# Kernel optimization log

Hardware: AMD Instinct MI355X
Metric: run time of the kernel (lower is better)

Reference implementation:

```python
import jax, jax.numpy as jnp
import numpy as np

B, S, H = 128, 1024, 256
NEG = 1e9

def setup_inputs() -> dict:
    key = jax.random.key(0)
    ks = jax.random.split(key, 11)
    sc = 0.05
    return {
        'ref': jax.random.normal(ks[0], (B, S, H), jnp.float32),
        'query': jax.random.normal(ks[1], (B, H), jnp.float32),
        'mask': jax.random.randint(ks[2], (B, S), 0, 2, jnp.int32),
        'wg': jax.random.normal(ks[3], (H, H), jnp.float32) * sc,
        'bg': jax.random.normal(ks[4], (H,), jnp.float32) * sc,
        'wqg': jax.random.normal(ks[5], (H, H), jnp.float32) * sc,
        'vg': jax.random.normal(ks[6], (H,), jnp.float32) * sc,
        'wp': jax.random.normal(ks[7], (H, H), jnp.float32) * sc,
        'bp': jax.random.normal(ks[8], (H,), jnp.float32) * sc,
        'wqp': jax.random.normal(ks[9], (H, H), jnp.float32) * sc,
        'vp': jax.random.normal(ks[10], (H,), jnp.float32) * sc,
    }

def reference(ref, query, mask, wg, bg, wqg, vg, wp, bp, wqp, vp):
    # Bahdanau additive pointer attention with glimpse, per PointerDecoder.pointer_net
    maskf = mask.astype(ref.dtype)
    # glimpse attention
    enc_g = jnp.einsum('bsd,hd->bsh', ref, wg) + bg            # conv1d kernel=1
    q_g = jnp.einsum('bd,hd->bh', query, wqg)                   # w_q_g (no bias)
    scores_g = jnp.einsum('bsh,h->bs', jnp.tanh(enc_g + q_g[:, None, :]), vg)
    att_g = jax.nn.softmax(scores_g - maskf * NEG, axis=-1)     # [B,S]
    glimpse = jnp.einsum('bs,bsd->bd', att_g, ref) + query      # [B,H]
    # pointer scores
    enc_p = jnp.einsum('bsd,hd->bsh', ref, wp) + bp
    q_p = jnp.einsum('bd,hd->bh', glimpse, wqp)
    scores_p = jnp.einsum('bsh,h->bs', jnp.tanh(enc_p + q_p[:, None, :]), vp)
    masked_scores = scores_p - maskf * NEG                      # [B,S]
    return masked_scores
```

## Files before the change

### kernel.cpp

```cpp
#include <hip/hip_runtime.h>

#define Bb 128
#define Ss 1024
#define Hh 256
#define NEGF 1e9f

typedef short bf16x8 __attribute__((ext_vector_type(8)));
typedef float f32x4 __attribute__((ext_vector_type(4)));

__device__ __forceinline__ short f2bf(float f) {
    union { float f; unsigned u; } c; c.f = f;
    return (short)((c.u + 0x8000u) >> 16);
}

__device__ __forceinline__ float bfhi2f(unsigned u) {
    union { unsigned u; float f; } c; c.u = u & 0xFFFF0000u; return c.f;
}
__device__ __forceinline__ float bflo2f(unsigned u) {
    union { unsigned u; float f; } c; c.u = u << 16; return c.f;
}

__device__ __forceinline__ float fast_tanh(float x) {
    float cl = fminf(fmaxf(x, -10.f), 10.f);
    float e = __expf(2.f * cl);
    return (e - 1.f) * __builtin_amdgcn_rcpf(e + 1.f);
}

__device__ __forceinline__ void stage16(const void* g, short* l) {
    __builtin_amdgcn_global_load_lds((const __attribute__((address_space(1))) void*)g,
                                     (__attribute__((address_space(3))) void*)l, 16, 0, 0);
}

#define WAITVM(N) { __builtin_amdgcn_s_waitcnt(0x0F70 | (N)); __builtin_amdgcn_sched_barrier(0); }

__global__ __launch_bounds__(256) void prep_kernel(const float* __restrict__ wg,
                                                   const float* __restrict__ wp,
                                                   const float* __restrict__ query,
                                                   const float* __restrict__ wqg,
                                                   const float* __restrict__ bg,
                                                   short* __restrict__ wgb,
                                                   short* __restrict__ wpb,
                                                   float* __restrict__ qbias_g) {
    int blk = blockIdx.x, t = threadIdx.x;
    if (blk < 256) {
        int i = blk * 256 + t;
        wgb[i] = f2bf(wg[i]);
        wpb[i] = f2bf(wp[i]);
    } else {
        int b = blk - 256;
        const float4* qr = (const float4*)(query + b * Hh);
        const float4* wr = (const float4*)(wqg + t * Hh);
        float acc = 0.f;
#pragma unroll 8
        for (int i = 0; i < Hh / 4; ++i) {
            float4 q4 = qr[i], w4 = wr[i];
            acc += q4.x * w4.x + q4.y * w4.y + q4.z * w4.z + q4.w * w4.w;
        }
        qbias_g[b * Hh + t] = acc + bg[t];
    }
}

template <int MASKED, int LOADF32>
__global__ __launch_bounds__(512, 2) void scores_mfma(const float* __restrict__ reff,
                                                      const short* __restrict__ refb_in,
                                                      short* __restrict__ refb_out,
                                                      const short* __restrict__ Wbf,
                                                      const float* __restrict__ qbias,
                                                      const float* __restrict__ vvec,
                                                      const int* __restrict__ mask,
                                                      float* __restrict__ out) {
    __shared__ __align__(16) short Abuf[2][8192];
    __shared__ float partial[8][256];
    const int t = threadIdx.x;
    const int w = t >> 6;
    const int lane = t & 63;
    const int nl = lane & 15;
    const int quad = lane >> 4;
    const int b = blockIdx.x >> 2;
    const int row0 = (blockIdx.x & 3) * 256;
    constexpr int I = LOADF32 ? 2 : 1;

    auto stage_tile = [&](int tt, int buf) {
        if (LOADF32) {
            const float* g = reff + ((size_t)b * Ss + row0 + tt * 16 + nl) * Hh + w * 32 + quad * 8;
            stage16(g,     &Abuf[buf][(w * 2 + 0) * 512]);
            stage16(g + 4, &Abuf[buf][(w * 2 + 1) * 512]);
        } else {
            const short* g = refb_in + ((size_t)b * Ss + row0 + tt * 16 + nl) * Hh + w * 32 + quad * 8;
            stage16(g, &Abuf[buf][w * 512]);
        }
    };

    stage_tile(0, 0);
    stage_tile(1, 1);

    bf16x8 bfrag[2][8];
#pragma unroll
    for (int nc2 = 0; nc2 < 2; ++nc2) {
        const short* wpr = Wbf + (w * 32 + nc2 * 16 + nl) * Hh + quad * 8;
#pragma unroll
        for (int kb = 0; kb < 8; ++kb)
            bfrag[nc2][kb] = *(const bf16x8*)(wpr + kb * 32);
    }
    const float qb0 = qbias[b * Hh + w * 32 + nl];
    const float qb1 = qbias[b * Hh + w * 32 + 16 + nl];
    const float vv0 = vvec[w * 32 + nl];
    const float vv1 = vvec[w * 32 + 16 + nl];

#pragma unroll 1
    for (int tt = 0; tt < 16; ++tt) {
        const int cur = tt & 1;
        if (tt < 15) WAITVM(I) else WAITVM(0)
        __builtin_amdgcn_s_barrier();
        __builtin_amdgcn_sched_barrier(0);

        const short* bufp = Abuf[cur];
        short* dst = refb_out + ((size_t)b * Ss + row0 + tt * 16 + nl) * Hh + quad * 8;
        const bool sideout = LOADF32 && ((tt & 7) == w);

        f32x4 c0 = {0.f, 0.f, 0.f, 0.f};
        f32x4 c1 = {0.f, 0.f, 0.f, 0.f};
#pragma unroll
        for (int kb = 0; kb < 8; ++kb) {
            bf16x8 af;
            if (LOADF32) {
                float4 lo = *(const float4*)&bufp[(kb * 2 + 0) * 512 + lane * 8];
                float4 hi = *(const float4*)&bufp[(kb * 2 + 1) * 512 + lane * 8];
                af[0] = f2bf(lo.x); af[1] = f2bf(lo.y); af[2] = f2bf(lo.z); af[3] = f2bf(lo.w);
                af[4] = f2bf(hi.x); af[5] = f2bf(hi.y); af[6] = f2bf(hi.z); af[7] = f2bf(hi.w);
                if (sideout) *(bf16x8*)(dst + kb * 32) = af;
            } else {
                af = *(const bf16x8*)&bufp[kb * 512 + lane * 8];
            }
            c0 = __builtin_amdgcn_mfma_f32_16x16x32_bf16(af, bfrag[0][kb], c0, 0, 0, 0);
            c1 = __builtin_amdgcn_mfma_f32_16x16x32_bf16(af, bfrag[1][kb], c1, 0, 0, 0);
        }
#pragma unroll
        for (int r = 0; r < 4; ++r) {
            float s = fast_tanh(c0[r] + qb0) * vv0 + fast_tanh(c1[r] + qb1) * vv1;
            s += __shfl_xor(s, 1, 64);
            s += __shfl_xor(s, 2, 64);
            s += __shfl_xor(s, 4, 64);
            s += __shfl_xor(s, 8, 64);
            if (nl == 0) partial[w][tt * 16 + quad * 4 + r] = s;
        }

        __builtin_amdgcn_s_barrier();
        __builtin_amdgcn_sched_barrier(0);
        if (tt < 14) stage_tile(tt + 2, cur);
    }

    __syncthreads();
    if (t < 256) {
        float s = 0.f;
#pragma unroll
        for (int g = 0; g < 8; ++g) s += partial[g][t];
        if (MASKED) s -= (float)mask[b * Ss + row0 + t] * NEGF;
        out[(size_t)b * Ss + row0 + t] = s;
    }
}

__global__ __launch_bounds__(1024) void softmax_kernel(const float* __restrict__ scores,
                                                       const int* __restrict__ mask,
                                                       float* __restrict__ att) {
    int b = blockIdx.x, t = threadIdx.x;
    __shared__ float red[16];
    int idx = b * Ss + t;
    float x = scores[idx] - (float)mask[idx] * NEGF;

    float m = x;
#pragma unroll
    for (int o = 1; o < 64; o <<= 1) m = fmaxf(m, __shfl_xor(m, o, 64));
    if ((t & 63) == 0) red[t >> 6] = m;
    __syncthreads();
    float M = red[0];
#pragma unroll
    for (int j = 1; j < 16; ++j) M = fmaxf(M, red[j]);
    __syncthreads();

    float e = __expf(x - M);
    float s = e;
#pragma unroll
    for (int o = 1; o < 64; o <<= 1) s += __shfl_xor(s, o, 64);
    if ((t & 63) == 0) red[t >> 6] = s;
    __syncthreads();
    float S = 0.f;
#pragma unroll
    for (int j = 0; j < 16; ++j) S += red[j];

    att[idx] = e * __builtin_amdgcn_rcpf(S);
}

__global__ __launch_bounds__(256) void glimpse_part(const unsigned* __restrict__ refb,
                                                    const float* __restrict__ att,
                                                    float* __restrict__ gpart) {
    int b = blockIdx.x, q = blockIdx.y, t = threadIdx.x;
    const int c = t & 31;
    const int rg = t >> 5;
    __shared__ float part[8][Hh];
    const unsigned* base = refb + ((size_t)(b * Ss + q * 128)) * (Hh / 2);
    const float* ap = att + b * Ss + q * 128;

    float acc[8] = {0.f, 0.f, 0.f, 0.f, 0.f, 0.f, 0.f, 0.f};
#pragma unroll 4
    for (int it = 0; it < 16; ++it) {
        int row = it * 8 + rg;
        float a = ap[row];
        uint4 v = *(const uint4*)(base + (size_t)row * (Hh / 2) + c * 4);
        acc[0] += a * bflo2f(v.x); acc[1] += a * bfhi2f(v.x);
        acc[2] += a * bflo2f(v.y); acc[3] += a * bfhi2f(v.y);
        acc[4] += a * bflo2f(v.z); acc[5] += a * bfhi2f(v.z);
        acc[6] += a * bflo2f(v.w); acc[7] += a * bfhi2f(v.w);
    }
#pragma unroll
    for (int j = 0; j < 8; ++j) part[rg][c * 8 + j] = acc[j];
    __syncthreads();
    float s = 0.f;
#pragma unroll
    for (int g = 0; g < 8; ++g) s += part[g][t];
    gpart[(size_t)(b * 8 + q) * Hh + t] = s;
}

__global__ __launch_bounds__(256) void qbias_p_kernel(const float* __restrict__ gpart,
                                                      const float* __restrict__ query,
                                                      const float* __restrict__ wqp,
                                                      const float* __restrict__ bp,
                                                      float* __restrict__ out) {
    int b = blockIdx.x, t = threadIdx.x;
    __shared__ __align__(16) float gl[Hh];
    float g = query[b * Hh + t];
#pragma unroll
    for (int q = 0; q < 8; ++q) g += gpart[(b * 8 + q) * Hh + t];
    gl[t] = g;
    __syncthreads();
    const float4* wr = (const float4*)(wqp + t * Hh);
    const float4* gp = (const float4*)gl;
    float acc = 0.f;
#pragma unroll 8
    for (int i = 0; i < Hh / 4; ++i) {
        float4 w4 = wr[i];
        float4 g4 = gp[i];
        acc += w4.x * g4.x + w4.y * g4.y + w4.z * g4.z + w4.w * g4.w;
    }
    out[b * Hh + t] = acc + bp[t];
}

extern "C" void kernel_launch(void* const* d_in, const int* in_sizes, int n_in,
                              void* d_out, int out_size, void* d_ws, size_t ws_size,
                              hipStream_t stream) {
    const float* ref   = (const float*)d_in[0];
    const float* query = (const float*)d_in[1];
    const int*   mask  = (const int*)d_in[2];
    const float* wg    = (const float*)d_in[3];
    const float* bg    = (const float*)d_in[4];
    const float* wqg   = (const float*)d_in[5];
    const float* vg    = (const float*)d_in[6];
    const float* wp    = (const float*)d_in[7];
    const float* bp    = (const float*)d_in[8];
    const float* wqp   = (const float*)d_in[9];
    const float* vp    = (const float*)d_in[10];
    float* out = (float*)d_out;

    char* ws = (char*)d_ws;
    short* ref_bf   = (short*)(ws + 0);
    size_t off = (size_t)Bb * Ss * Hh * 2;
    short* wg_bf    = (short*)(ws + off);               off += 131072;
    short* wp_bf    = (short*)(ws + off);               off += 131072;
    float* qbias_g  = (float*)(ws + off);               off += 131072;
    float* qbias_p  = (float*)(ws + off);               off += 131072;
    float* scores_g = (float*)(ws + off);               off += 524288;
    float* att      = (float*)(ws + off);               off += 524288;
    float* gpart    = (float*)(ws + off);

    prep_kernel<<<384, 256, 0, stream>>>(wg, wp, query, wqg, bg, wg_bf, wp_bf, qbias_g);
    scores_mfma<0, 1><<<512, 512, 0, stream>>>(
        ref, nullptr, ref_bf, wg_bf, qbias_g, vg, nullptr, scores_g);
    softmax_kernel<<<Bb, Ss, 0, stream>>>(scores_g, mask, att);
    glimpse_part<<<dim3(Bb, 8), 256, 0, stream>>>((const unsigned*)ref_bf, att, gpart);
    qbias_p_kernel<<<Bb, Hh, 0, stream>>>(gpart, query, wqp, bp, qbias_p);
    scores_mfma<1, 0><<<512, 512, 0, stream>>>(
        nullptr, ref_bf, nullptr, wp_bf, qbias_p, vp, mask, out);
}
```

Before: 293.3 us.

## Deepen scores pipeline to 4 buffers and move bf16 ref cast into glimpse

The MFMA scores kernel now uses a four-slot LDS ring with prefetch depth three. It issues the next stage right after the barrier, which drops the second per-iteration barrier. The fp32-to-bf16 copy of ref is no longer written by the first scores kernel; glimpse_part now reads fp32 ref directly, accumulates in fp32 and emits the bf16 copy. Conversions use the packed hardware bf16 convert instruction. This lightens the first GEMM kernel and improves its latency hiding, but it adds extra fp32 reads in glimpse and doubles LDS use per block.

```diff
diff --git a/kernel.cpp b/kernel.cpp
--- a/kernel.cpp
+++ b/kernel.cpp
@@ -13,11 +13,10 @@
     return (short)((c.u + 0x8000u) >> 16);
 }
 
-__device__ __forceinline__ float bfhi2f(unsigned u) {
-    union { unsigned u; float f; } c; c.u = u & 0xFFFF0000u; return c.f;
-}
-__device__ __forceinline__ float bflo2f(unsigned u) {
-    union { unsigned u; float f; } c; c.u = u << 16; return c.f;
+__device__ __forceinline__ unsigned cvt_pk_bf16(float a, float b) {
+    unsigned r;
+    asm("v_cvt_pk_bf16_f32 %0, %1, %2" : "=v"(r) : "v"(a), "v"(b));
+    return r;
 }
 
 __device__ __forceinline__ float fast_tanh(float x) {
@@ -63,13 +62,14 @@
 template <int MASKED, int LOADF32>
 __global__ __launch_bounds__(512, 2) void scores_mfma(const float* __restrict__ reff,
                                                       const short* __restrict__ refb_in,
-                                                      short* __restrict__ refb_out,
                                                       const short* __restrict__ Wbf,
                                                       const float* __restrict__ qbias,
                                                       const float* __restrict__ vvec,
                                                       const int* __restrict__ mask,
                                                       float* __restrict__ out) {
-    __shared__ __align__(16) short Abuf[2][8192];
+    constexpr int TS = LOADF32 ? 8192 : 4096;
+    constexpr int I = LOADF32 ? 2 : 1;
+    __shared__ __align__(16) short Abuf[4][TS];
     __shared__ float partial[8][256];
     const int t = threadIdx.x;
     const int w = t >> 6;
@@ -78,7 +78,19 @@
     const int quad = lane >> 4;
     const int b = blockIdx.x >> 2;
     const int row0 = (blockIdx.x & 3) * 256;
-    constexpr int I = LOADF32 ? 2 : 1;
+
+    bf16x8 bfrag[2][8];
+#pragma unroll
+    for (int nc2 = 0; nc2 < 2; ++nc2) {
+        const short* wpr = Wbf + (w * 32 + nc2 * 16 + nl) * Hh + quad * 8;
+#pragma unroll
+        for (int kb = 0; kb < 8; ++kb)
+            bfrag[nc2][kb] = *(const bf16x8*)(wpr + kb * 32);
+    }
+    const float qb0 = qbias[b * Hh + w * 32 + nl];
+    const float qb1 = qbias[b * Hh + w * 32 + 16 + nl];
+    const float vv0 = vvec[w * 32 + nl];
+    const float vv1 = vvec[w * 32 + 16 + nl];
 
     auto stage_tile = [&](int tt, int buf) {
         if (LOADF32) {
@@ -93,31 +105,18 @@
 
     stage_tile(0, 0);
     stage_tile(1, 1);
-
-    bf16x8 bfrag[2][8];
-#pragma unroll
-    for (int nc2 = 0; nc2 < 2; ++nc2) {
-        const short* wpr = Wbf + (w * 32 + nc2 * 16 + nl) * Hh + quad * 8;
-#pragma unroll
-        for (int kb = 0; kb < 8; ++kb)
-            bfrag[nc2][kb] = *(const bf16x8*)(wpr + kb * 32);
-    }
-    const float qb0 = qbias[b * Hh + w * 32 + nl];
-    const float qb1 = qbias[b * Hh + w * 32 + 16 + nl];
-    const float vv0 = vvec[w * 32 + nl];
-    const float vv1 = vvec[w * 32 + 16 + nl];
+    stage_tile(2, 2);
 
 #pragma unroll 1
     for (int tt = 0; tt < 16; ++tt) {
-        const int cur = tt & 1;
-        if (tt < 15) WAITVM(I) else WAITVM(0)
+        if (tt <= 13)      WAITVM(2 * I)
+        else if (tt == 14) WAITVM(I)
+        else               WAITVM(0)
         __builtin_amdgcn_s_barrier();
         __builtin_amdgcn_sched_barrier(0);
-
-        const short* bufp = Abuf[cur];
-        short* dst = refb_out + ((size_t)b * Ss + row0 + tt * 16 + nl) * Hh + quad * 8;
-        const bool sideout = LOADF32 && ((tt & 7) == w);
-
+        if (tt <= 12) stage_tile(tt + 3, (tt + 3) & 3);
+
+        const short* bufp = Abuf[tt & 3];
         f32x4 c0 = {0.f, 0.f, 0.f, 0.f};
         f32x4 c1 = {0.f, 0.f, 0.f, 0.f};
 #pragma unroll
@@ -126,9 +125,12 @@
             if (LOADF32) {
                 float4 lo = *(const float4*)&bufp[(kb * 2 + 0) * 512 + lane * 8];
                 float4 hi = *(const float4*)&bufp[(kb * 2 + 1) * 512 + lane * 8];
-                af[0] = f2bf(lo.x); af[1] = f2bf(lo.y); af[2] = f2bf(lo.z); af[3] = f2bf(lo.w);
-                af[4] = f2bf(hi.x); af[5] = f2bf(hi.y); af[6] = f2bf(hi.z); af[7] = f2bf(hi.w);
-                if (sideout) *(bf16x8*)(dst + kb * 32) = af;
+                union { unsigned u[4]; bf16x8 v; } cv;
+                cv.u[0] = cvt_pk_bf16(lo.x, lo.y);
+                cv.u[1] = cvt_pk_bf16(lo.z, lo.w);
+                cv.u[2] = cvt_pk_bf16(hi.x, hi.y);
+                cv.u[3] = cvt_pk_bf16(hi.z, hi.w);
+                af = cv.v;
             } else {
                 af = *(const bf16x8*)&bufp[kb * 512 + lane * 8];
             }
@@ -144,10 +146,6 @@
             s += __shfl_xor(s, 8, 64);
             if (nl == 0) partial[w][tt * 16 + quad * 4 + r] = s;
         }
-
-        __builtin_amdgcn_s_barrier();
-        __builtin_amdgcn_sched_barrier(0);
-        if (tt < 14) stage_tile(tt + 2, cur);
     }
 
     __syncthreads();
@@ -191,14 +189,16 @@
     att[idx] = e * __builtin_amdgcn_rcpf(S);
 }
 
-__global__ __launch_bounds__(256) void glimpse_part(const unsigned* __restrict__ refb,
+__global__ __launch_bounds__(256) void glimpse_part(const float* __restrict__ reff,
                                                     const float* __restrict__ att,
+                                                    short* __restrict__ refb_out,
                                                     float* __restrict__ gpart) {
     int b = blockIdx.x, q = blockIdx.y, t = threadIdx.x;
     const int c = t & 31;
     const int rg = t >> 5;
     __shared__ float part[8][Hh];
-    const unsigned* base = refb + ((size_t)(b * Ss + q * 128)) * (Hh / 2);
+    const float* base = reff + ((size_t)(b * Ss + q * 128)) * Hh;
+    short* outb = refb_out + ((size_t)(b * Ss + q * 128)) * Hh;
     const float* ap = att + b * Ss + q * 128;
 
     float acc[8] = {0.f, 0.f, 0.f, 0.f, 0.f, 0.f, 0.f, 0.f};
@@ -206,11 +206,16 @@
     for (int it = 0; it < 16; ++it) {
         int row = it * 8 + rg;
         float a = ap[row];
-        uint4 v = *(const uint4*)(base + (size_t)row * (Hh / 2) + c * 4);
-        acc[0] += a * bflo2f(v.x); acc[1] += a * bfhi2f(v.x);
-        acc[2] += a * bflo2f(v.y); acc[3] += a * bfhi2f(v.y);
-        acc[4] += a * bflo2f(v.z); acc[5] += a * bfhi2f(v.z);
-        acc[6] += a * bflo2f(v.w); acc[7] += a * bfhi2f(v.w);
+        const float4* rp = (const float4*)(base + (size_t)row * Hh + c * 8);
+        float4 lo = rp[0], hi = rp[1];
+        acc[0] += a * lo.x; acc[1] += a * lo.y; acc[2] += a * lo.z; acc[3] += a * lo.w;
+        acc[4] += a * hi.x; acc[5] += a * hi.y; acc[6] += a * hi.z; acc[7] += a * hi.w;
+        union { unsigned u[4]; bf16x8 v; } cv;
+        cv.u[0] = cvt_pk_bf16(lo.x, lo.y);
+        cv.u[1] = cvt_pk_bf16(lo.z, lo.w);
+        cv.u[2] = cvt_pk_bf16(hi.x, hi.y);
+        cv.u[3] = cvt_pk_bf16(hi.z, hi.w);
+        *(bf16x8*)(outb + (size_t)row * Hh + c * 8) = cv.v;
     }
 #pragma unroll
     for (int j = 0; j < 8; ++j) part[rg][c * 8 + j] = acc[j];
@@ -274,10 +279,10 @@
 
     prep_kernel<<<384, 256, 0, stream>>>(wg, wp, query, wqg, bg, wg_bf, wp_bf, qbias_g);
     scores_mfma<0, 1><<<512, 512, 0, stream>>>(
-        ref, nullptr, ref_bf, wg_bf, qbias_g, vg, nullptr, scores_g);
+        ref, nullptr, wg_bf, qbias_g, vg, nullptr, scores_g);
     softmax_kernel<<<Bb, Ss, 0, stream>>>(scores_g, mask, att);
-    glimpse_part<<<dim3(Bb, 8), 256, 0, stream>>>((const unsigned*)ref_bf, att, gpart);
+    glimpse_part<<<dim3(Bb, 8), 256, 0, stream>>>(ref, att, ref_bf, gpart);
     qbias_p_kernel<<<Bb, Hh, 0, stream>>>(gpart, query, wqp, bp, qbias_p);
     scores_mfma<1, 0><<<512, 512, 0, stream>>>(
-        nullptr, ref_bf, nullptr, wp_bf, qbias_p, vp, mask, out);
-}
+        nullptr, ref_bf, wp_bf, qbias_p, vp, mask, out);
+}
```

After: 304.3 us. +3.8%, slower.
